# Optimization experiments

Hardware: AMD Instinct MI355X
Metric: run time of the kernel (lower is better)

Reference implementation:

```python
import jax, jax.numpy as jnp
import numpy as np

B, H, IN, T = 32768, 128, 128, 10
SPARSITY = 0.8


def setup_inputs() -> dict:
    key = jax.random.key(0)
    ks = jax.random.split(key, 12)
    x = jax.random.normal(ks[0], (B, IN), dtype=jnp.float32)
    hidden = jax.random.normal(ks[1], (B, H), dtype=jnp.float32)
    time_span = jnp.linspace(0.0, 1.0, T).astype(jnp.float32)
    # sparse binary wiring mask: rand < 1 - sparsity (WiringType.ADAPTIVE default branch)
    wiring = (jax.random.uniform(ks[2], (H, H)) < (1.0 - SPARSITY)).astype(jnp.float32)
    W = jax.random.normal(ks[3], (H, H), dtype=jnp.float32) * 0.1
    b = jnp.zeros((H,), dtype=jnp.float32)
    W_in = jax.random.normal(ks[4], (H, IN), dtype=jnp.float32) / np.sqrt(IN)
    b_in = jnp.zeros((H,), dtype=jnp.float32)
    W_upd = jax.random.normal(ks[5], (H, H + IN), dtype=jnp.float32) / np.sqrt(H + IN)
    b_upd = jnp.zeros((H,), dtype=jnp.float32)
    W_rst = jax.random.normal(ks[6], (H, H + IN), dtype=jnp.float32) / np.sqrt(H + IN)
    b_rst = jnp.zeros((H,), dtype=jnp.float32)
    return dict(x=x, hidden=hidden, time_span=time_span, wiring=wiring, W=W, b=b,
                W_in=W_in, b_in=b_in, W_upd=W_upd, b_upd=b_upd, W_rst=W_rst, b_rst=b_rst)


def reference(x, hidden, time_span, wiring, W, b, W_in, b_in, W_upd, b_upd, W_rst, b_rst):
    # input projection and GRU-style gates on [hidden, x]
    x_proj = x @ W_in.T + b_in                                   # [B, H]
    combined = jnp.concatenate([hidden, x], axis=1)              # [B, H+IN]
    update = jax.nn.sigmoid(combined @ W_upd.T + b_upd)          # [B, H]
    reset = jax.nn.sigmoid(combined @ W_rst.T + b_rst)           # [B, H]
    h0 = reset * hidden                                          # [B, H]

    W_eff_T = (W * wiring).T                                     # [H, H], masked recurrent weights

    def f(h):
        # dh/dt = -h + tanh(W_eff h + b) + x_proj  (tau = 1.0: config has no log_tau attr)
        return -h + jnp.tanh(h @ W_eff_T + b) + x_proj

    def rk4_step(h, dt):
        k1 = f(h)
        k2 = f(h + 0.5 * dt * k1)
        k3 = f(h + 0.5 * dt * k2)
        k4 = f(h + dt * k3)
        h_new = h + (dt / 6.0) * (k1 + 2.0 * k2 + 2.0 * k3 + k4)
        return h_new, h_new

    dts = jnp.diff(time_span)                                    # [T-1]
    h_last, traj = jax.lax.scan(rk4_step, h0, dts)               # traj: [T-1, B, H]
    ode_out = jnp.concatenate([h0[None], traj], axis=0)          # [T, B, H]
    new_hidden = update * h_last + (1.0 - update) * h0           # [B, H]
    return new_hidden, ode_out
```

## Files before the change

### kernel.cpp

```cpp
#include <hip/hip_runtime.h>


constexpr int kB   = 32768;
constexpr int kH   = 128;
constexpr int kIn  = 128;
constexpr int kT   = 10;
constexpr int ROWS = 64;
constexpr int NT   = ROWS / 16;
constexpr int LDSW = 136;
constexpr int HIN  = 256;

typedef __bf16 bf16;
typedef __attribute__((ext_vector_type(8))) __bf16 bf16x8;
typedef __attribute__((ext_vector_type(4))) __bf16 bf16x4;
typedef __attribute__((ext_vector_type(4))) float  f32x4;

__device__ __forceinline__ float sigmoid_(float v) {
  return __fdividef(1.0f, 1.0f + __expf(-v));
}
__device__ __forceinline__ float tanh_(float v) {
  float e = __expf(2.0f * v);
  return 1.0f - __fdividef(2.0f, 1.0f + e);
}

__device__ __forceinline__ bf16x8 cvt8(const float* p) {
  float4 f0 = *(const float4*)p;
  float4 f1 = *(const float4*)(p + 4);
  bf16x8 t;
  t[0]=(bf16)f0.x; t[1]=(bf16)f0.y; t[2]=(bf16)f0.z; t[3]=(bf16)f0.w;
  t[4]=(bf16)f1.x; t[5]=(bf16)f1.y; t[6]=(bf16)f1.z; t[7]=(bf16)f1.w;
  return t;
}

__device__ __forceinline__ void gemm4(
    f32x4 (&C)[NT], const bf16 (*S)[LDSW],
    const float* __restrict__ Wb, int ldw, int kofs,
    int wave, int quad, int l16)
{
#pragma unroll
  for (int kk = 0; kk < 4; ++kk) {
    bf16x8 af = cvt8(Wb + (size_t)(wave*16 + l16) * ldw + kofs + kk*32 + quad*8);
#pragma unroll
    for (int nt = 0; nt < NT; ++nt) {
      bf16x8 bfv = *(const bf16x8*)&S[nt*16 + l16][kk*32 + quad*8];
      C[nt] = __builtin_amdgcn_mfma_f32_16x16x32_bf16(af, bfv, C[nt], 0, 0, 0);
    }
  }
}

__device__ __forceinline__ void feval(
    f32x4 (&K)[NT], const bf16x8 (&weff)[4], const bf16 (*Y)[LDSW],
    float4 bv, int quad, int l16)
{
#pragma unroll
  for (int nt = 0; nt < NT; ++nt)
    K[nt] = f32x4{bv.x, bv.y, bv.z, bv.w};
#pragma unroll
  for (int kk = 0; kk < 4; ++kk)
#pragma unroll
    for (int nt = 0; nt < NT; ++nt) {
      bf16x8 bfv = *(const bf16x8*)&Y[nt*16 + l16][kk*32 + quad*8];
      K[nt] = __builtin_amdgcn_mfma_f32_16x16x32_bf16(weff[kk], bfv, K[nt], 0, 0, 0);
    }
}

__device__ __forceinline__ void storeTile(
    bf16 (*Y)[LDSW], const f32x4 (&V)[NT], int hc0, int l16)
{
#pragma unroll
  for (int nt = 0; nt < NT; ++nt) {
    bf16x4 p;
    p[0]=(bf16)V[nt][0]; p[1]=(bf16)V[nt][1];
    p[2]=(bf16)V[nt][2]; p[3]=(bf16)V[nt][3];
    *(bf16x4*)&Y[nt*16 + l16][hc0] = p;
  }
}

__device__ __forceinline__ void storeGlob(
    float* gbase, const f32x4 (&V)[NT], int hc0, int l16)
{
#pragma unroll
  for (int nt = 0; nt < NT; ++nt) {
    float4 g{V[nt][0], V[nt][1], V[nt][2], V[nt][3]};
    *(float4*)(gbase + (size_t)(nt*16 + l16) * kH + hc0) = g;
  }
}

__global__ __launch_bounds__(512, 4) void ltc_kernel(
    const float* __restrict__ x,     const float* __restrict__ hidden,
    const float* __restrict__ ts,    const float* __restrict__ wiring,
    const float* __restrict__ W,     const float* __restrict__ bb_,
    const float* __restrict__ W_in,  const float* __restrict__ b_in,
    const float* __restrict__ W_upd, const float* __restrict__ b_upd,
    const float* __restrict__ W_rst, const float* __restrict__ b_rst,
    float* __restrict__ out)
{
  __shared__ bf16 ldsX [ROWS][LDSW];
  __shared__ bf16 ldsHd[ROWS][LDSW];
  __shared__ bf16 ldsY0[ROWS][LDSW];
  __shared__ bf16 ldsY1[ROWS][LDSW];
  __shared__ float sts[kT];

  const int tid  = threadIdx.x;
  const int wave = tid >> 6;
  const int lane = tid & 63;
  const int quad = lane >> 4;
  const int l16  = lane & 15;
  const int r0   = blockIdx.x * ROWS;

  if (tid < kT) sts[tid] = ts[tid];

#pragma unroll
  for (int i = 0; i < 4; ++i) {
    int idx = i*512 + tid;
    int row = idx >> 5;
    int c4  = (idx & 31) * 4;
    float4 vx = *(const float4*)(x      + (size_t)(r0+row)*kIn + c4);
    float4 vh = *(const float4*)(hidden + (size_t)(r0+row)*kH  + c4);
    bf16x4 bx; bx[0]=(bf16)vx.x; bx[1]=(bf16)vx.y; bx[2]=(bf16)vx.z; bx[3]=(bf16)vx.w;
    bf16x4 bh; bh[0]=(bf16)vh.x; bh[1]=(bf16)vh.y; bh[2]=(bf16)vh.z; bh[3]=(bf16)vh.w;
    *(bf16x4*)&ldsX [row][c4] = bx;
    *(bf16x4*)&ldsHd[row][c4] = bh;
  }

  const int hc0 = wave*16 + quad*4;

  bf16x8 weff[4];
  {
    int hrow = wave*16 + l16;
#pragma unroll
    for (int kk = 0; kk < 4; ++kk) {
      int k = kk*32 + quad*8;
      const float* wp = W      + (size_t)hrow*kH + k;
      const float* mp = wiring + (size_t)hrow*kH + k;
      float4 w0 = *(const float4*)wp, w1 = *(const float4*)(wp+4);
      float4 m0 = *(const float4*)mp, m1 = *(const float4*)(mp+4);
      bf16x8 t;
      t[0]=(bf16)(w0.x*m0.x); t[1]=(bf16)(w0.y*m0.y);
      t[2]=(bf16)(w0.z*m0.z); t[3]=(bf16)(w0.w*m0.w);
      t[4]=(bf16)(w1.x*m1.x); t[5]=(bf16)(w1.y*m1.y);
      t[6]=(bf16)(w1.z*m1.z); t[7]=(bf16)(w1.w*m1.w);
      weff[kk] = t;
    }
  }
  float4 bv = *(const float4*)(bb_ + hc0);

  __syncthreads();

  f32x4 xp[NT];
  {
    float4 bi = *(const float4*)(b_in + hc0);
#pragma unroll
    for (int nt = 0; nt < NT; ++nt)
      xp[nt] = f32x4{bi.x, bi.y, bi.z, bi.w};
    gemm4(xp, ldsX, W_in, kIn, 0, wave, quad, l16);
  }

  f32x4 h[NT], U[NT];
  {
    f32x4 R[NT];
    float4 br = *(const float4*)(b_rst + hc0);
    float4 bu = *(const float4*)(b_upd + hc0);
#pragma unroll
    for (int nt = 0; nt < NT; ++nt) {
      R[nt] = f32x4{br.x, br.y, br.z, br.w};
      U[nt] = f32x4{bu.x, bu.y, bu.z, bu.w};
    }
    gemm4(R, ldsHd, W_rst, HIN, 0,  wave, quad, l16);
    gemm4(R, ldsX,  W_rst, HIN, kH, wave, quad, l16);
    gemm4(U, ldsHd, W_upd, HIN, 0,  wave, quad, l16);
    gemm4(U, ldsX,  W_upd, HIN, kH, wave, quad, l16);

#pragma unroll
    for (int nt = 0; nt < NT; ++nt) {
      const float* hp = hidden + (size_t)(r0 + nt*16 + l16)*kH + hc0;
      float4 hv = *(const float4*)hp;
      h[nt][0] = sigmoid_(R[nt][0]) * hv.x;
      h[nt][1] = sigmoid_(R[nt][1]) * hv.y;
      h[nt][2] = sigmoid_(R[nt][2]) * hv.z;
      h[nt][3] = sigmoid_(R[nt][3]) * hv.w;
      U[nt][0] = sigmoid_(U[nt][0]);
      U[nt][1] = sigmoid_(U[nt][1]);
      U[nt][2] = sigmoid_(U[nt][2]);
      U[nt][3] = sigmoid_(U[nt][3]);
    }
  }

  __syncthreads();

  storeTile(ldsHd, U, hc0, l16);
  storeTile(ldsX,  h, hc0, l16);
  storeTile(ldsY0, h, hc0, l16);

  f32x4 z[NT], hacc[NT], K[NT];
#pragma unroll
  for (int nt = 0; nt < NT; ++nt) z[nt] = h[nt];

  float* odeBase = out + (size_t)kB*kH + (size_t)r0*kH;

  for (int t = 1; t < kT; ++t) {
    float dt  = sts[t] - sts[t-1];
    float dt6 = dt * (1.0f/6.0f);
    float dt3 = dt * (1.0f/3.0f);
    float dth = 0.5f * dt;

    __syncthreads();
    storeGlob(odeBase + (size_t)(t-1)*kB*kH, h, hc0, l16);
    feval(K, weff, ldsY0, bv, quad, l16);
#pragma unroll
    for (int nt = 0; nt < NT; ++nt)
#pragma unroll
      for (int i = 0; i < 4; ++i) {
        float kv = tanh_(K[nt][i]) + xp[nt][i] - z[nt][i];
        hacc[nt][i] = h[nt][i] + dt6 * kv;
        z[nt][i]    = h[nt][i] + dth * kv;
      }
    storeTile(ldsY1, z, hc0, l16);

    __syncthreads();
    feval(K, weff, ldsY1, bv, quad, l16);
#pragma unroll
    for (int nt = 0; nt < NT; ++nt)
#pragma unroll
      for (int i = 0; i < 4; ++i) {
        float kv = tanh_(K[nt][i]) + xp[nt][i] - z[nt][i];
        hacc[nt][i] += dt3 * kv;
        z[nt][i]     = h[nt][i] + dth * kv;
      }
    storeTile(ldsY0, z, hc0, l16);

    __syncthreads();
    feval(K, weff, ldsY0, bv, quad, l16);
#pragma unroll
    for (int nt = 0; nt < NT; ++nt)
#pragma unroll
      for (int i = 0; i < 4; ++i) {
        float kv = tanh_(K[nt][i]) + xp[nt][i] - z[nt][i];
        hacc[nt][i] += dt3 * kv;
        z[nt][i]     = h[nt][i] + dt * kv;
      }
    storeTile(ldsY1, z, hc0, l16);

    __syncthreads();
    feval(K, weff, ldsY1, bv, quad, l16);
#pragma unroll
    for (int nt = 0; nt < NT; ++nt)
#pragma unroll
      for (int i = 0; i < 4; ++i) {
        float kv = tanh_(K[nt][i]) + xp[nt][i] - z[nt][i];
        h[nt][i] = hacc[nt][i] + dt6 * kv;
        z[nt][i] = h[nt][i];
      }
    storeTile(ldsY0, z, hc0, l16);
  }

  storeGlob(odeBase + (size_t)(kT-1)*kB*kH, h, hc0, l16);

#pragma unroll
  for (int nt = 0; nt < NT; ++nt) {
    int r = nt*16 + l16;
    bf16x4 uv  = *(const bf16x4*)&ldsHd[r][hc0];
    bf16x4 h0v = *(const bf16x4*)&ldsX [r][hc0];
    float4 p;
    {
      float uu;
      uu = (float)uv[0]; p.x = uu * h[nt][0] + (1.0f - uu) * (float)h0v[0];
      uu = (float)uv[1]; p.y = uu * h[nt][1] + (1.0f - uu) * (float)h0v[1];
      uu = (float)uv[2]; p.z = uu * h[nt][2] + (1.0f - uu) * (float)h0v[2];
      uu = (float)uv[3]; p.w = uu * h[nt][3] + (1.0f - uu) * (float)h0v[3];
    }
    *(float4*)(out + (size_t)(r0 + r) * kH + hc0) = p;
  }
}

extern "C" void kernel_launch(void* const* d_in, const int* in_sizes, int n_in,
                              void* d_out, int out_size, void* d_ws, size_t ws_size,
                              hipStream_t stream) {
  (void)d_ws; (void)ws_size; (void)out_size;
  int ix=0, ih=1, its=2, iwr=3, iW=4, ib=5, iWin=6, ibin=7, iWu=8, ibu=9, iWr=10, ibr=11;
  if (n_in == 12 && in_sizes[2] != 10 && in_sizes[5] == 10) {
    ib=0; ibin=1; ibr=2; ibu=3; ih=4; its=5; iW=6; iWin=7; iWr=8; iWu=9; iwr=10; ix=11;
  }
  const float* x      = (const float*)d_in[ix];
  const float* hidden = (const float*)d_in[ih];
  const float* ts     = (const float*)d_in[its];
  const float* wiring = (const float*)d_in[iwr];
  const float* W      = (const float*)d_in[iW];
  const float* b      = (const float*)d_in[ib];
  const float* W_in   = (const float*)d_in[iWin];
  const float* b_in   = (const float*)d_in[ibin];
  const float* W_upd  = (const float*)d_in[iWu];
  const float* b_upd  = (const float*)d_in[ibu];
  const float* W_rst  = (const float*)d_in[iWr];
  const float* b_rst  = (const float*)d_in[ibr];

  dim3 grid(kB / ROWS);
  dim3 block(512);
  ltc_kernel<<<grid, block, 0, stream>>>(x, hidden, ts, wiring, W, b,
                                         W_in, b_in, W_upd, b_upd, W_rst, b_rst,
                                         (float*)d_out);
}
```

Measured before the change: 347.5 us.

## Split each block's rows across two wave groups using 1024-thread blocks

Doubles the threads per block to 16 waves. Each wave now handles one 16-column H tile for half of the 64 rows (NT=2) instead of all 64 rows. The goal is more waves per block to hide latency and fewer registers per thread, allowing higher occupancy. The cost is that each W_eff fragment and weight load is duplicated across two waves, and more threads take part in each __syncthreads.

```diff
diff --git a/kernel.cpp b/kernel.cpp
--- a/kernel.cpp
+++ b/kernel.cpp
@@ -6,7 +6,7 @@
 constexpr int kIn  = 128;
 constexpr int kT   = 10;
 constexpr int ROWS = 64;
-constexpr int NT   = ROWS / 16;
+constexpr int NT   = 2;
 constexpr int LDSW = 136;
 constexpr int HIN  = 256;
 
@@ -35,14 +35,14 @@
 __device__ __forceinline__ void gemm4(
     f32x4 (&C)[NT], const bf16 (*S)[LDSW],
     const float* __restrict__ Wb, int ldw, int kofs,
-    int wave, int quad, int l16)
+    int hTile, int rbase, int quad, int l16)
 {
 #pragma unroll
   for (int kk = 0; kk < 4; ++kk) {
-    bf16x8 af = cvt8(Wb + (size_t)(wave*16 + l16) * ldw + kofs + kk*32 + quad*8);
+    bf16x8 af = cvt8(Wb + (size_t)(hTile*16 + l16) * ldw + kofs + kk*32 + quad*8);
 #pragma unroll
     for (int nt = 0; nt < NT; ++nt) {
-      bf16x8 bfv = *(const bf16x8*)&S[nt*16 + l16][kk*32 + quad*8];
+      bf16x8 bfv = *(const bf16x8*)&S[rbase + nt*16 + l16][kk*32 + quad*8];
       C[nt] = __builtin_amdgcn_mfma_f32_16x16x32_bf16(af, bfv, C[nt], 0, 0, 0);
     }
   }
@@ -50,7 +50,7 @@
 
 __device__ __forceinline__ void feval(
     f32x4 (&K)[NT], const bf16x8 (&weff)[4], const bf16 (*Y)[LDSW],
-    float4 bv, int quad, int l16)
+    float4 bv, int rbase, int quad, int l16)
 {
 #pragma unroll
   for (int nt = 0; nt < NT; ++nt)
@@ -59,34 +59,34 @@
   for (int kk = 0; kk < 4; ++kk)
 #pragma unroll
     for (int nt = 0; nt < NT; ++nt) {
-      bf16x8 bfv = *(const bf16x8*)&Y[nt*16 + l16][kk*32 + quad*8];
+      bf16x8 bfv = *(const bf16x8*)&Y[rbase + nt*16 + l16][kk*32 + quad*8];
       K[nt] = __builtin_amdgcn_mfma_f32_16x16x32_bf16(weff[kk], bfv, K[nt], 0, 0, 0);
     }
 }
 
 __device__ __forceinline__ void storeTile(
-    bf16 (*Y)[LDSW], const f32x4 (&V)[NT], int hc0, int l16)
+    bf16 (*Y)[LDSW], const f32x4 (&V)[NT], int hc0, int rbase, int l16)
 {
 #pragma unroll
   for (int nt = 0; nt < NT; ++nt) {
     bf16x4 p;
     p[0]=(bf16)V[nt][0]; p[1]=(bf16)V[nt][1];
     p[2]=(bf16)V[nt][2]; p[3]=(bf16)V[nt][3];
-    *(bf16x4*)&Y[nt*16 + l16][hc0] = p;
+    *(bf16x4*)&Y[rbase + nt*16 + l16][hc0] = p;
   }
 }
 
 __device__ __forceinline__ void storeGlob(
-    float* gbase, const f32x4 (&V)[NT], int hc0, int l16)
+    float* gbase, const f32x4 (&V)[NT], int hc0, int rbase, int l16)
 {
 #pragma unroll
   for (int nt = 0; nt < NT; ++nt) {
     float4 g{V[nt][0], V[nt][1], V[nt][2], V[nt][3]};
-    *(float4*)(gbase + (size_t)(nt*16 + l16) * kH + hc0) = g;
-  }
-}
-
-__global__ __launch_bounds__(512, 4) void ltc_kernel(
+    *(float4*)(gbase + (size_t)(rbase + nt*16 + l16) * kH + hc0) = g;
+  }
+}
+
+__global__ __launch_bounds__(1024, 8) void ltc_kernel(
     const float* __restrict__ x,     const float* __restrict__ hidden,
     const float* __restrict__ ts,    const float* __restrict__ wiring,
     const float* __restrict__ W,     const float* __restrict__ bb_,
@@ -101,18 +101,20 @@
   __shared__ bf16 ldsY1[ROWS][LDSW];
   __shared__ float sts[kT];
 
-  const int tid  = threadIdx.x;
-  const int wave = tid >> 6;
-  const int lane = tid & 63;
-  const int quad = lane >> 4;
-  const int l16  = lane & 15;
-  const int r0   = blockIdx.x * ROWS;
+  const int tid   = threadIdx.x;
+  const int wave  = tid >> 6;
+  const int hTile = wave & 7;
+  const int rbase = (wave >> 3) * 32;
+  const int lane  = tid & 63;
+  const int quad  = lane >> 4;
+  const int l16   = lane & 15;
+  const int r0    = blockIdx.x * ROWS;
 
   if (tid < kT) sts[tid] = ts[tid];
 
 #pragma unroll
-  for (int i = 0; i < 4; ++i) {
-    int idx = i*512 + tid;
+  for (int i = 0; i < 2; ++i) {
+    int idx = i*1024 + tid;
     int row = idx >> 5;
     int c4  = (idx & 31) * 4;
     float4 vx = *(const float4*)(x      + (size_t)(r0+row)*kIn + c4);
@@ -123,11 +125,11 @@
     *(bf16x4*)&ldsHd[row][c4] = bh;
   }
 
-  const int hc0 = wave*16 + quad*4;
+  const int hc0 = hTile*16 + quad*4;
 
   bf16x8 weff[4];
   {
-    int hrow = wave*16 + l16;
+    int hrow = hTile*16 + l16;
 #pragma unroll
     for (int kk = 0; kk < 4; ++kk) {
       int k = kk*32 + quad*8;
@@ -153,7 +155,7 @@
 #pragma unroll
     for (int nt = 0; nt < NT; ++nt)
       xp[nt] = f32x4{bi.x, bi.y, bi.z, bi.w};
-    gemm4(xp, ldsX, W_in, kIn, 0, wave, quad, l16);
+    gemm4(xp, ldsX, W_in, kIn, 0, hTile, rbase, quad, l16);
   }
 
   f32x4 h[NT], U[NT];
@@ -166,14 +168,14 @@
       R[nt] = f32x4{br.x, br.y, br.z, br.w};
       U[nt] = f32x4{bu.x, bu.y, bu.z, bu.w};
     }
-    gemm4(R, ldsHd, W_rst, HIN, 0,  wave, quad, l16);
-    gemm4(R, ldsX,  W_rst, HIN, kH, wave, quad, l16);
-    gemm4(U, ldsHd, W_upd, HIN, 0,  wave, quad, l16);
-    gemm4(U, ldsX,  W_upd, HIN, kH, wave, quad, l16);
+    gemm4(R, ldsHd, W_rst, HIN, 0,  hTile, rbase, quad, l16);
+    gemm4(R, ldsX,  W_rst, HIN, kH, hTile, rbase, quad, l16);
+    gemm4(U, ldsHd, W_upd, HIN, 0,  hTile, rbase, quad, l16);
+    gemm4(U, ldsX,  W_upd, HIN, kH, hTile, rbase, quad, l16);
 
 #pragma unroll
     for (int nt = 0; nt < NT; ++nt) {
-      const float* hp = hidden + (size_t)(r0 + nt*16 + l16)*kH + hc0;
+      const float* hp = hidden + (size_t)(r0 + rbase + nt*16 + l16)*kH + hc0;
       float4 hv = *(const float4*)hp;
       h[nt][0] = sigmoid_(R[nt][0]) * hv.x;
       h[nt][1] = sigmoid_(R[nt][1]) * hv.y;
@@ -188,9 +190,9 @@
 
   __syncthreads();
 
-  storeTile(ldsHd, U, hc0, l16);
-  storeTile(ldsX,  h, hc0, l16);
-  storeTile(ldsY0, h, hc0, l16);
+  storeTile(ldsHd, U, hc0, rbase, l16);
+  storeTile(ldsX,  h, hc0, rbase, l16);
+  storeTile(ldsY0, h, hc0, rbase, l16);
 
   f32x4 z[NT], hacc[NT], K[NT];
 #pragma unroll
@@ -205,8 +207,8 @@
     float dth = 0.5f * dt;
 
     __syncthreads();
-    storeGlob(odeBase + (size_t)(t-1)*kB*kH, h, hc0, l16);
-    feval(K, weff, ldsY0, bv, quad, l16);
+    storeGlob(odeBase + (size_t)(t-1)*kB*kH, h, hc0, rbase, l16);
+    feval(K, weff, ldsY0, bv, rbase, quad, l16);
 #pragma unroll
     for (int nt = 0; nt < NT; ++nt)
 #pragma unroll
@@ -215,10 +217,10 @@
         hacc[nt][i] = h[nt][i] + dt6 * kv;
         z[nt][i]    = h[nt][i] + dth * kv;
       }
-    storeTile(ldsY1, z, hc0, l16);
+    storeTile(ldsY1, z, hc0, rbase, l16);
 
     __syncthreads();
-    feval(K, weff, ldsY1, bv, quad, l16);
+    feval(K, weff, ldsY1, bv, rbase, quad, l16);
 #pragma unroll
     for (int nt = 0; nt < NT; ++nt)
 #pragma unroll
@@ -227,10 +229,10 @@
         hacc[nt][i] += dt3 * kv;
         z[nt][i]     = h[nt][i] + dth * kv;
       }
-    storeTile(ldsY0, z, hc0, l16);
+    storeTile(ldsY0, z, hc0, rbase, l16);
 
     __syncthreads();
-    feval(K, weff, ldsY0, bv, quad, l16);
+    feval(K, weff, ldsY0, bv, rbase, quad, l16);
 #pragma unroll
     for (int nt = 0; nt < NT; ++nt)
 #pragma unroll
@@ -239,10 +241,10 @@
         hacc[nt][i] += dt3 * kv;
         z[nt][i]     = h[nt][i] + dt * kv;
       }
-    storeTile(ldsY1, z, hc0, l16);
+    storeTile(ldsY1, z, hc0, rbase, l16);
 
     __syncthreads();
-    feval(K, weff, ldsY1, bv, quad, l16);
+    feval(K, weff, ldsY1, bv, rbase, quad, l16);
 #pragma unroll
     for (int nt = 0; nt < NT; ++nt)
 #pragma unroll
@@ -251,14 +253,14 @@
         h[nt][i] = hacc[nt][i] + dt6 * kv;
         z[nt][i] = h[nt][i];
       }
-    storeTile(ldsY0, z, hc0, l16);
-  }
-
-  storeGlob(odeBase + (size_t)(kT-1)*kB*kH, h, hc0, l16);
+    storeTile(ldsY0, z, hc0, rbase, l16);
+  }
+
+  storeGlob(odeBase + (size_t)(kT-1)*kB*kH, h, hc0, rbase, l16);
 
 #pragma unroll
   for (int nt = 0; nt < NT; ++nt) {
-    int r = nt*16 + l16;
+    int r = rbase + nt*16 + l16;
     bf16x4 uv  = *(const bf16x4*)&ldsHd[r][hc0];
     bf16x4 h0v = *(const bf16x4*)&ldsX [r][hc0];
     float4 p;
@@ -295,7 +297,7 @@
   const float* b_rst  = (const float*)d_in[ibr];
 
   dim3 grid(kB / ROWS);
-  dim3 block(512);
+  dim3 block(1024);
   ltc_kernel<<<grid, block, 0, stream>>>(x, hidden, ts, wiring, W, b,
                                          W_in, b_in, W_upd, b_upd, W_rst, b_rst,
                                          (float*)d_out);
```

After: 541.4 us. 1.56x slower.

## Give each wave its own batch rows to drop per-stage block barriers

Applied to the files above, without the earlier changes.

Work is now split by batch rows instead of hidden columns. Each of 4 waves owns 16 rows and all 128 hidden outputs, so the RK4 stages only exchange data within a wave and the __syncthreads between stages are gone. The masked recurrent weights are staged once in LDS as MFMA fragments and reread on every evaluation. Gate GEMMs keep the combined input in registers, and tanh uses exp2/rcp intrinsics. The cost is many more accumulator registers per lane (launch bounds drop to 256 threads, 2 blocks) and extra LDS reads of the weights per stage.

```diff
diff --git a/kernel.cpp b/kernel.cpp
--- a/kernel.cpp
+++ b/kernel.cpp
@@ -6,9 +6,10 @@
 constexpr int kIn  = 128;
 constexpr int kT   = 10;
 constexpr int ROWS = 64;
-constexpr int NT   = ROWS / 16;
+constexpr int RW   = 16;
 constexpr int LDSW = 136;
 constexpr int HIN  = 256;
+constexpr int NHT  = 8;
 
 typedef __bf16 bf16;
 typedef __attribute__((ext_vector_type(8))) __bf16 bf16x8;
@@ -17,10 +18,6 @@
 
 __device__ __forceinline__ float sigmoid_(float v) {
   return __fdividef(1.0f, 1.0f + __expf(-v));
-}
-__device__ __forceinline__ float tanh_(float v) {
-  float e = __expf(2.0f * v);
-  return 1.0f - __fdividef(2.0f, 1.0f + e);
 }
 
 __device__ __forceinline__ bf16x8 cvt8(const float* p) {
@@ -32,61 +29,7 @@
   return t;
 }
 
-__device__ __forceinline__ void gemm4(
-    f32x4 (&C)[NT], const bf16 (*S)[LDSW],
-    const float* __restrict__ Wb, int ldw, int kofs,
-    int wave, int quad, int l16)
-{
-#pragma unroll
-  for (int kk = 0; kk < 4; ++kk) {
-    bf16x8 af = cvt8(Wb + (size_t)(wave*16 + l16) * ldw + kofs + kk*32 + quad*8);
-#pragma unroll
-    for (int nt = 0; nt < NT; ++nt) {
-      bf16x8 bfv = *(const bf16x8*)&S[nt*16 + l16][kk*32 + quad*8];
-      C[nt] = __builtin_amdgcn_mfma_f32_16x16x32_bf16(af, bfv, C[nt], 0, 0, 0);
-    }
-  }
-}
-
-__device__ __forceinline__ void feval(
-    f32x4 (&K)[NT], const bf16x8 (&weff)[4], const bf16 (*Y)[LDSW],
-    float4 bv, int quad, int l16)
-{
-#pragma unroll
-  for (int nt = 0; nt < NT; ++nt)
-    K[nt] = f32x4{bv.x, bv.y, bv.z, bv.w};
-#pragma unroll
-  for (int kk = 0; kk < 4; ++kk)
-#pragma unroll
-    for (int nt = 0; nt < NT; ++nt) {
-      bf16x8 bfv = *(const bf16x8*)&Y[nt*16 + l16][kk*32 + quad*8];
-      K[nt] = __builtin_amdgcn_mfma_f32_16x16x32_bf16(weff[kk], bfv, K[nt], 0, 0, 0);
-    }
-}
-
-__device__ __forceinline__ void storeTile(
-    bf16 (*Y)[LDSW], const f32x4 (&V)[NT], int hc0, int l16)
-{
-#pragma unroll
-  for (int nt = 0; nt < NT; ++nt) {
-    bf16x4 p;
-    p[0]=(bf16)V[nt][0]; p[1]=(bf16)V[nt][1];
-    p[2]=(bf16)V[nt][2]; p[3]=(bf16)V[nt][3];
-    *(bf16x4*)&Y[nt*16 + l16][hc0] = p;
-  }
-}
-
-__device__ __forceinline__ void storeGlob(
-    float* gbase, const f32x4 (&V)[NT], int hc0, int l16)
-{
-#pragma unroll
-  for (int nt = 0; nt < NT; ++nt) {
-    float4 g{V[nt][0], V[nt][1], V[nt][2], V[nt][3]};
-    *(float4*)(gbase + (size_t)(nt*16 + l16) * kH + hc0) = g;
-  }
-}
-
-__global__ __launch_bounds__(512, 4) void ltc_kernel(
+__global__ __launch_bounds__(256, 2) void ltc_kernel(
     const float* __restrict__ x,     const float* __restrict__ hidden,
     const float* __restrict__ ts,    const float* __restrict__ wiring,
     const float* __restrict__ W,     const float* __restrict__ bb_,
@@ -95,181 +38,215 @@
     const float* __restrict__ W_rst, const float* __restrict__ b_rst,
     float* __restrict__ out)
 {
-  __shared__ bf16 ldsX [ROWS][LDSW];
-  __shared__ bf16 ldsHd[ROWS][LDSW];
-  __shared__ bf16 ldsY0[ROWS][LDSW];
-  __shared__ bf16 ldsY1[ROWS][LDSW];
-  __shared__ float sts[kT];
+  __shared__ bf16 poolX [ROWS][LDSW];
+  __shared__ bf16 poolHd[ROWS][LDSW];
+  __shared__ bf16 weffF[32][64][8];
+  __shared__ float sbias[kH];
+  __shared__ float stsv[kT];
 
   const int tid  = threadIdx.x;
-  const int wave = tid >> 6;
+  const int wv   = tid >> 6;
   const int lane = tid & 63;
-  const int quad = lane >> 4;
+  const int qd   = lane >> 4;
   const int l16  = lane & 15;
   const int r0   = blockIdx.x * ROWS;
-
-  if (tid < kT) sts[tid] = ts[tid];
-
-#pragma unroll
-  for (int i = 0; i < 4; ++i) {
-    int idx = i*512 + tid;
+  const int rbase = wv * RW;
+  const int grow  = r0 + rbase + l16;
+
+  if (tid < kT) stsv[tid] = ts[tid];
+  if (tid < kH) sbias[tid] = bb_[tid];
+
+#pragma unroll
+  for (int i = 0; i < 8; ++i) {
+    int idx = i*256 + tid;
     int row = idx >> 5;
     int c4  = (idx & 31) * 4;
     float4 vx = *(const float4*)(x      + (size_t)(r0+row)*kIn + c4);
     float4 vh = *(const float4*)(hidden + (size_t)(r0+row)*kH  + c4);
     bf16x4 bx; bx[0]=(bf16)vx.x; bx[1]=(bf16)vx.y; bx[2]=(bf16)vx.z; bx[3]=(bf16)vx.w;
     bf16x4 bh; bh[0]=(bf16)vh.x; bh[1]=(bf16)vh.y; bh[2]=(bf16)vh.z; bh[3]=(bf16)vh.w;
-    *(bf16x4*)&ldsX [row][c4] = bx;
-    *(bf16x4*)&ldsHd[row][c4] = bh;
-  }
-
-  const int hc0 = wave*16 + quad*4;
-
-  bf16x8 weff[4];
-  {
-    int hrow = wave*16 + l16;
-#pragma unroll
-    for (int kk = 0; kk < 4; ++kk) {
-      int k = kk*32 + quad*8;
-      const float* wp = W      + (size_t)hrow*kH + k;
-      const float* mp = wiring + (size_t)hrow*kH + k;
-      float4 w0 = *(const float4*)wp, w1 = *(const float4*)(wp+4);
-      float4 m0 = *(const float4*)mp, m1 = *(const float4*)(mp+4);
-      bf16x8 t;
-      t[0]=(bf16)(w0.x*m0.x); t[1]=(bf16)(w0.y*m0.y);
-      t[2]=(bf16)(w0.z*m0.z); t[3]=(bf16)(w0.w*m0.w);
-      t[4]=(bf16)(w1.x*m1.x); t[5]=(bf16)(w1.y*m1.y);
-      t[6]=(bf16)(w1.z*m1.z); t[7]=(bf16)(w1.w*m1.w);
-      weff[kk] = t;
+    *(bf16x4*)&poolX [row][c4] = bx;
+    *(bf16x4*)&poolHd[row][c4] = bh;
+  }
+
+#pragma unroll
+  for (int j = 0; j < 8; ++j) {
+    int f = wv*8 + j, ht = f >> 2, kk = f & 3;
+    const float* wp = W      + (size_t)(ht*16 + l16)*kH + kk*32 + qd*8;
+    const float* mp = wiring + (size_t)(ht*16 + l16)*kH + kk*32 + qd*8;
+    float4 w0 = *(const float4*)wp, w1 = *(const float4*)(wp+4);
+    float4 m0 = *(const float4*)mp, m1 = *(const float4*)(mp+4);
+    bf16x8 t;
+    t[0]=(bf16)(w0.x*m0.x); t[1]=(bf16)(w0.y*m0.y);
+    t[2]=(bf16)(w0.z*m0.z); t[3]=(bf16)(w0.w*m0.w);
+    t[4]=(bf16)(w1.x*m1.x); t[5]=(bf16)(w1.y*m1.y);
+    t[6]=(bf16)(w1.z*m1.z); t[7]=(bf16)(w1.w*m1.w);
+    *(bf16x8*)&weffF[f][lane][0] = t;
+  }
+  __syncthreads();
+
+  bf16x8 cb[8];
+#pragma unroll
+  for (int kk = 0; kk < 4; ++kk)
+    cb[kk]   = *(const bf16x8*)&poolHd[rbase + l16][kk*32 + qd*8];
+#pragma unroll
+  for (int kk = 0; kk < 4; ++kk)
+    cb[4+kk] = *(const bf16x8*)&poolX [rbase + l16][kk*32 + qd*8];
+
+  f32x4 XP[NHT], Ug[NHT], Rg[NHT];
+#pragma unroll
+  for (int ht = 0; ht < NHT; ++ht) {
+    float4 bi = *(const float4*)(b_in  + 16*ht + 4*qd);
+    float4 bu = *(const float4*)(b_upd + 16*ht + 4*qd);
+    float4 br = *(const float4*)(b_rst + 16*ht + 4*qd);
+    XP[ht] = f32x4{bi.x, bi.y, bi.z, bi.w};
+    Ug[ht] = f32x4{bu.x, bu.y, bu.z, bu.w};
+    Rg[ht] = f32x4{br.x, br.y, br.z, br.w};
+  }
+#pragma unroll
+  for (int ht = 0; ht < NHT; ++ht) {
+    const float* wu = W_upd + (size_t)(16*ht + l16)*HIN + qd*8;
+    const float* wr = W_rst + (size_t)(16*ht + l16)*HIN + qd*8;
+#pragma unroll
+    for (int kk = 0; kk < 8; ++kk) {
+      Ug[ht] = __builtin_amdgcn_mfma_f32_16x16x32_bf16(cvt8(wu + kk*32), cb[kk], Ug[ht], 0,0,0);
+      Rg[ht] = __builtin_amdgcn_mfma_f32_16x16x32_bf16(cvt8(wr + kk*32), cb[kk], Rg[ht], 0,0,0);
     }
-  }
-  float4 bv = *(const float4*)(bb_ + hc0);
-
+    const float* wi = W_in + (size_t)(16*ht + l16)*kIn + qd*8;
+#pragma unroll
+    for (int kk = 0; kk < 4; ++kk)
+      XP[ht] = __builtin_amdgcn_mfma_f32_16x16x32_bf16(cvt8(wi + kk*32), cb[4+kk], XP[ht], 0,0,0);
+  }
+
+  f32x4 h[NHT], z[NHT], hacc[NHT], xp1[NHT], K[NHT];
+  bf16x4 ub[NHT], h0b[NHT];
+#pragma unroll
+  for (int ht = 0; ht < NHT; ++ht) {
+    float4 hv = *(const float4*)(hidden + (size_t)grow*kH + 16*ht + 4*qd);
+    h[ht][0] = sigmoid_(Rg[ht][0]) * hv.x;
+    h[ht][1] = sigmoid_(Rg[ht][1]) * hv.y;
+    h[ht][2] = sigmoid_(Rg[ht][2]) * hv.z;
+    h[ht][3] = sigmoid_(Rg[ht][3]) * hv.w;
+#pragma unroll
+    for (int i = 0; i < 4; ++i) {
+      ub[ht][i]  = (bf16)sigmoid_(Ug[ht][i]);
+      h0b[ht][i] = (bf16)h[ht][i];
+      xp1[ht][i] = XP[ht][i] + 1.0f;
+      z[ht][i]   = h[ht][i];
+    }
+  }
   __syncthreads();
 
-  f32x4 xp[NT];
-  {
-    float4 bi = *(const float4*)(b_in + hc0);
-#pragma unroll
-    for (int nt = 0; nt < NT; ++nt)
-      xp[nt] = f32x4{bi.x, bi.y, bi.z, bi.w};
-    gemm4(xp, ldsX, W_in, kIn, 0, wave, quad, l16);
-  }
-
-  f32x4 h[NT], U[NT];
-  {
-    f32x4 R[NT];
-    float4 br = *(const float4*)(b_rst + hc0);
-    float4 bu = *(const float4*)(b_upd + hc0);
-#pragma unroll
-    for (int nt = 0; nt < NT; ++nt) {
-      R[nt] = f32x4{br.x, br.y, br.z, br.w};
-      U[nt] = f32x4{bu.x, bu.y, bu.z, bu.w};
+  bf16 (*zt)[LDSW] = (bf16 (*)[LDSW])&poolX[rbase][0];
+  float* odeB = out + (size_t)kB*kH;
+
+#pragma unroll
+  for (int ht = 0; ht < NHT; ++ht) {
+    bf16x4 p;
+    p[0]=(bf16)h[ht][0]; p[1]=(bf16)h[ht][1]; p[2]=(bf16)h[ht][2]; p[3]=(bf16)h[ht][3];
+    *(bf16x4*)&zt[l16][16*ht + 4*qd] = p;
+    *(f32x4*)(odeB + (size_t)grow*kH + 16*ht + 4*qd) = h[ht];
+  }
+  bf16x8 zf[4];
+#pragma unroll
+  for (int kk = 0; kk < 4; ++kk)
+    zf[kk] = *(const bf16x8*)&zt[l16][kk*32 + qd*8];
+
+  auto feval = [&]() {
+#pragma unroll
+    for (int ht = 0; ht < NHT; ++ht)
+      K[ht] = *(const f32x4*)&sbias[16*ht + 4*qd];
+#pragma unroll
+    for (int kk = 0; kk < 4; ++kk)
+#pragma unroll
+      for (int ht = 0; ht < NHT; ++ht) {
+        bf16x8 wf = *(const bf16x8*)&weffF[ht*4 + kk][lane][0];
+        K[ht] = __builtin_amdgcn_mfma_f32_16x16x32_bf16(wf, zf[kk], K[ht], 0,0,0);
+      }
+  };
+  auto zwrite = [&]() {
+#pragma unroll
+    for (int ht = 0; ht < NHT; ++ht) {
+      bf16x4 p;
+      p[0]=(bf16)z[ht][0]; p[1]=(bf16)z[ht][1]; p[2]=(bf16)z[ht][2]; p[3]=(bf16)z[ht][3];
+      *(bf16x4*)&zt[l16][16*ht + 4*qd] = p;
     }
-    gemm4(R, ldsHd, W_rst, HIN, 0,  wave, quad, l16);
-    gemm4(R, ldsX,  W_rst, HIN, kH, wave, quad, l16);
-    gemm4(U, ldsHd, W_upd, HIN, 0,  wave, quad, l16);
-    gemm4(U, ldsX,  W_upd, HIN, kH, wave, quad, l16);
-
-#pragma unroll
-    for (int nt = 0; nt < NT; ++nt) {
-      const float* hp = hidden + (size_t)(r0 + nt*16 + l16)*kH + hc0;
-      float4 hv = *(const float4*)hp;
-      h[nt][0] = sigmoid_(R[nt][0]) * hv.x;
-      h[nt][1] = sigmoid_(R[nt][1]) * hv.y;
-      h[nt][2] = sigmoid_(R[nt][2]) * hv.z;
-      h[nt][3] = sigmoid_(R[nt][3]) * hv.w;
-      U[nt][0] = sigmoid_(U[nt][0]);
-      U[nt][1] = sigmoid_(U[nt][1]);
-      U[nt][2] = sigmoid_(U[nt][2]);
-      U[nt][3] = sigmoid_(U[nt][3]);
-    }
-  }
-
-  __syncthreads();
-
-  storeTile(ldsHd, U, hc0, l16);
-  storeTile(ldsX,  h, hc0, l16);
-  storeTile(ldsY0, h, hc0, l16);
-
-  f32x4 z[NT], hacc[NT], K[NT];
-#pragma unroll
-  for (int nt = 0; nt < NT; ++nt) z[nt] = h[nt];
-
-  float* odeBase = out + (size_t)kB*kH + (size_t)r0*kH;
+#pragma unroll
+    for (int kk = 0; kk < 4; ++kk)
+      zf[kk] = *(const bf16x8*)&zt[l16][kk*32 + qd*8];
+  };
+  auto kvf = [&](int ht, int i) -> float {
+    float m = 2.8853900817779268f * K[ht][i];
+    float e = __builtin_amdgcn_exp2f(m);
+    float r = __builtin_amdgcn_rcpf(1.0f + e);
+    return __builtin_fmaf(-2.0f, r, xp1[ht][i] - z[ht][i]);
+  };
 
   for (int t = 1; t < kT; ++t) {
-    float dt  = sts[t] - sts[t-1];
-    float dt6 = dt * (1.0f/6.0f);
-    float dt3 = dt * (1.0f/3.0f);
-    float dth = 0.5f * dt;
-
-    __syncthreads();
-    storeGlob(odeBase + (size_t)(t-1)*kB*kH, h, hc0, l16);
-    feval(K, weff, ldsY0, bv, quad, l16);
-#pragma unroll
-    for (int nt = 0; nt < NT; ++nt)
-#pragma unroll
-      for (int i = 0; i < 4; ++i) {
-        float kv = tanh_(K[nt][i]) + xp[nt][i] - z[nt][i];
-        hacc[nt][i] = h[nt][i] + dt6 * kv;
-        z[nt][i]    = h[nt][i] + dth * kv;
-      }
-    storeTile(ldsY1, z, hc0, l16);
-
-    __syncthreads();
-    feval(K, weff, ldsY1, bv, quad, l16);
-#pragma unroll
-    for (int nt = 0; nt < NT; ++nt)
-#pragma unroll
-      for (int i = 0; i < 4; ++i) {
-        float kv = tanh_(K[nt][i]) + xp[nt][i] - z[nt][i];
-        hacc[nt][i] += dt3 * kv;
-        z[nt][i]     = h[nt][i] + dth * kv;
-      }
-    storeTile(ldsY0, z, hc0, l16);
-
-    __syncthreads();
-    feval(K, weff, ldsY0, bv, quad, l16);
-#pragma unroll
-    for (int nt = 0; nt < NT; ++nt)
-#pragma unroll
-      for (int i = 0; i < 4; ++i) {
-        float kv = tanh_(K[nt][i]) + xp[nt][i] - z[nt][i];
-        hacc[nt][i] += dt3 * kv;
-        z[nt][i]     = h[nt][i] + dt * kv;
-      }
-    storeTile(ldsY1, z, hc0, l16);
-
-    __syncthreads();
-    feval(K, weff, ldsY1, bv, quad, l16);
-#pragma unroll
-    for (int nt = 0; nt < NT; ++nt)
-#pragma unroll
-      for (int i = 0; i < 4; ++i) {
-        float kv = tanh_(K[nt][i]) + xp[nt][i] - z[nt][i];
-        h[nt][i] = hacc[nt][i] + dt6 * kv;
-        z[nt][i] = h[nt][i];
-      }
-    storeTile(ldsY0, z, hc0, l16);
-  }
-
-  storeGlob(odeBase + (size_t)(kT-1)*kB*kH, h, hc0, l16);
-
-#pragma unroll
-  for (int nt = 0; nt < NT; ++nt) {
-    int r = nt*16 + l16;
-    bf16x4 uv  = *(const bf16x4*)&ldsHd[r][hc0];
-    bf16x4 h0v = *(const bf16x4*)&ldsX [r][hc0];
+    float dt = stsv[t] - stsv[t-1];
+    float c6 = dt * (1.0f/6.0f);
+    float c3 = dt * (1.0f/3.0f);
+    float ch = 0.5f * dt;
+
+    feval();
+#pragma unroll
+    for (int ht = 0; ht < NHT; ++ht)
+#pragma unroll
+      for (int i = 0; i < 4; ++i) {
+        float kv = kvf(ht, i);
+        hacc[ht][i] = __builtin_fmaf(c6, kv, h[ht][i]);
+        z[ht][i]    = __builtin_fmaf(ch, kv, h[ht][i]);
+      }
+    zwrite();
+
+    feval();
+#pragma unroll
+    for (int ht = 0; ht < NHT; ++ht)
+#pragma unroll
+      for (int i = 0; i < 4; ++i) {
+        float kv = kvf(ht, i);
+        hacc[ht][i] = __builtin_fmaf(c3, kv, hacc[ht][i]);
+        z[ht][i]    = __builtin_fmaf(ch, kv, h[ht][i]);
+      }
+    zwrite();
+
+    feval();
+#pragma unroll
+    for (int ht = 0; ht < NHT; ++ht)
+#pragma unroll
+      for (int i = 0; i < 4; ++i) {
+        float kv = kvf(ht, i);
+        hacc[ht][i] = __builtin_fmaf(c3, kv, hacc[ht][i]);
+        z[ht][i]    = __builtin_fmaf(dt, kv, h[ht][i]);
+      }
+    zwrite();
+
+    feval();
+#pragma unroll
+    for (int ht = 0; ht < NHT; ++ht)
+#pragma unroll
+      for (int i = 0; i < 4; ++i) {
+        float kv = kvf(ht, i);
+        h[ht][i] = __builtin_fmaf(c6, kv, hacc[ht][i]);
+        z[ht][i] = h[ht][i];
+      }
+    zwrite();
+
+    float* odet = odeB + (size_t)t*kB*kH + (size_t)grow*kH;
+#pragma unroll
+    for (int ht = 0; ht < NHT; ++ht)
+      *(f32x4*)(odet + 16*ht + 4*qd) = h[ht];
+  }
+
+#pragma unroll
+  for (int ht = 0; ht < NHT; ++ht) {
     float4 p;
-    {
-      float uu;
-      uu = (float)uv[0]; p.x = uu * h[nt][0] + (1.0f - uu) * (float)h0v[0];
-      uu = (float)uv[1]; p.y = uu * h[nt][1] + (1.0f - uu) * (float)h0v[1];
-      uu = (float)uv[2]; p.z = uu * h[nt][2] + (1.0f - uu) * (float)h0v[2];
-      uu = (float)uv[3]; p.w = uu * h[nt][3] + (1.0f - uu) * (float)h0v[3];
-    }
-    *(float4*)(out + (size_t)(r0 + r) * kH + hc0) = p;
+    float uu;
+    uu=(float)ub[ht][0]; p.x = uu*h[ht][0] + (1.0f-uu)*(float)h0b[ht][0];
+    uu=(float)ub[ht][1]; p.y = uu*h[ht][1] + (1.0f-uu)*(float)h0b[ht][1];
+    uu=(float)ub[ht][2]; p.z = uu*h[ht][2] + (1.0f-uu)*(float)h0b[ht][2];
+    uu=(float)ub[ht][3]; p.w = uu*h[ht][3] + (1.0f-uu)*(float)h0b[ht][3];
+    *(float4*)(out + (size_t)grow*kH + 16*ht + 4*qd) = p;
   }
 }
 
@@ -295,7 +272,7 @@
   const float* b_rst  = (const float*)d_in[ibr];
 
   dim3 grid(kB / ROWS);
-  dim3 block(512);
+  dim3 block(256);
   ltc_kernel<<<grid, block, 0, stream>>>(x, hidden, ts, wiring, W, b,
                                          W_in, b_in, W_upd, b_upd, W_rst, b_rst,
                                          (float*)d_out);
```

Result: slower. 686.6 us (+97.6%).
